# Kernel optimization log

Measured on AMD Instinct MI355X. Metric: run time of the kernel, lower is better.

The kernel has to match this reference:

```python
import jax, jax.numpy as jnp
import numpy as np

N = 50000      # nodes
E = 800000     # edges (avg degree 16)
IN, EMB, HID, OUT = 128, 256, 256, 128
KS = (25000, 12500)  # absolute top-k node counts per pooling level
NEG = -1e9


def setup_inputs() -> dict:
    key = jax.random.key(0)
    k = jax.random.split(key, 20)
    s = 0.05
    rn = lambda kk, shp: (jax.random.normal(kk, shp, jnp.float32) * s)
    return {
        "features": jax.random.normal(k[0], (N, IN), jnp.float32),
        "src": jax.random.randint(k[1], (E,), 0, N, dtype=jnp.int32),
        "dst": jax.random.randint(k[2], (E,), 0, N, dtype=jnp.int32),
        "W_embed": rn(k[3], (IN, EMB)), "b_embed": jnp.zeros((EMB,), jnp.float32),
        "W_enc0": rn(k[4], (EMB, HID)), "b_enc0": jnp.zeros((HID,), jnp.float32),
        "W_enc1": rn(k[5], (HID, HID)), "b_enc1": jnp.zeros((HID,), jnp.float32),
        "W_p0": rn(k[6], (HID, 1)), "b_p0": jnp.zeros((1,), jnp.float32),
        "W_p1": rn(k[7], (HID, 1)), "b_p1": jnp.zeros((1,), jnp.float32),
        "W_bot": rn(k[8], (HID, HID)), "b_bot": jnp.zeros((HID,), jnp.float32),
        "W_dec0": rn(k[9], (HID, HID)), "b_dec0": jnp.zeros((HID,), jnp.float32),
        "W_dec1": rn(k[10], (HID, OUT)), "b_dec1": jnp.zeros((OUT,), jnp.float32),
    }


def _gcn(h, src, dst, emask, W, b, act):
    """DGL GraphConv, norm='both': D_out^{-1/2} A D_in^{-1/2} h W + b, deg clamped >=1.
    emask: float [E] validity mask for edges of the current (sub)graph."""
    n = h.shape[0]
    deg_out = jnp.clip(jax.ops.segment_sum(emask, src, num_segments=n), 1.0)
    deg_in = jnp.clip(jax.ops.segment_sum(emask, dst, num_segments=n), 1.0)
    msg = (h * (deg_out ** -0.5)[:, None])[src] * emask[:, None]  # [E, F]
    agg = jax.ops.segment_sum(msg, dst, num_segments=n)
    out = (agg * (deg_in ** -0.5)[:, None]) @ W + b
    return jax.nn.relu(out) if act else out


def _forward(features, src, dst, W_embed, b_embed, W_enc0, b_enc0, W_enc1, b_enc1,
             W_p0, b_p0, W_p1, b_p1, W_bot, b_bot, W_dec0, b_dec0, W_dec1, b_dec1):
    n = features.shape[0]
    ones_e = jnp.ones((src.shape[0],), features.dtype)
    enc = [(W_enc0, b_enc0), (W_enc1, b_enc1)]
    pools = [(W_p0, b_p0), (W_p1, b_p1)]
    dec = [(W_dec0, b_dec0), (W_dec1, b_dec1)]
    L = len(KS)

    h = _gcn(features, src, dst, ones_e, W_embed, b_embed, True)
    masks = [jnp.ones((n,), features.dtype)]  # node mask per graph level
    hidden = []
    for i in range(L):  # encoder (dropout = eval-mode identity)
        m = masks[i]
        em = m[src] * m[dst]
        h = _gcn(h, src, dst, em, enc[i][0], enc[i][1], True) * m[:, None]
        hidden.append(h)
        # gPool: sigmoid projection score, top-k node selection, gate by score
        scores = jax.nn.sigmoid(h @ pools[i][0] + pools[i][1])[:, 0]
        _, idx = jax.lax.top_k(jnp.where(m > 0, scores, NEG), KS[i])
        nm = jnp.zeros((n,), features.dtype).at[idx].set(1.0)
        h = h * (scores * nm)[:, None]
        masks.append(nm)
    mL = masks[L]
    emL = mL[src] * mL[dst]
    h = _gcn(h, src, dst, emL, W_bot, b_bot, True) * mL[:, None]
    for i in range(L):  # decoder: gUnpool (identity under full-rep masking) + skip + GCN
        j = L - 1 - i
        h = h + hidden[j]
        m = masks[j]
        em = m[src] * m[dst]
        act = i < L - 1  # last decoder layer has no activation
        h = _gcn(h, src, dst, em, dec[i][0], dec[i][1], act) * m[:, None]
    return h


def reference(features, src, dst, W_embed, b_embed, W_enc0, b_enc0, W_enc1, b_enc1,
              W_p0, b_p0, W_p1, b_p1, W_bot, b_bot, W_dec0, b_dec0, W_dec1, b_dec1):
    return _forward(features, src, dst, W_embed, b_embed, W_enc0, b_enc0, W_enc1, b_enc1,
                    W_p0, b_p0, W_p1, b_p1, W_bot, b_bot, W_dec0, b_dec0, W_dec1, b_dec1)
```

## Files before the change

### kernel.cpp

```cpp
#include <hip/hip_runtime.h>
#include <hip/hip_bf16.h>
#include <type_traits>

__global__ void hist_kernel(const int* __restrict__ src, const int* __restrict__ dst,
                            int* __restrict__ deg_out, int* __restrict__ deg_in, int E) {
    int e = blockIdx.x * blockDim.x + threadIdx.x;
    if (e < E) {
        atomicAdd(&deg_out[src[e]], 1);
        atomicAdd(&deg_in[dst[e]], 1);
    }
}

__global__ void scan_kernel(const int* __restrict__ deg, int* __restrict__ row_ptr,
                            int* __restrict__ cursor, int n) {
    __shared__ int wsum[16];
    __shared__ int running;
    int tid = threadIdx.x, lane = tid & 63, wid = tid >> 6;
    if (tid == 0) running = 0;
    __syncthreads();
    for (int base = 0; base < n; base += 1024) {
        int i = base + tid;
        int v = (i < n) ? deg[i] : 0;
        int incl = v;
        #pragma unroll
// ... 93 lines not shown
__device__ __forceinline__ void split4(float x, float y, float z, float w,
                                       ushort4& hv, ushort4& lv) {
    hv.x = f2bf(x); lv.x = f2bf(x - bf2f(hv.x));
    hv.y = f2bf(y); lv.y = f2bf(y - bf2f(hv.y));
    hv.z = f2bf(z); lv.z = f2bf(z - bf2f(hv.z));
    hv.w = f2bf(w); lv.w = f2bf(w - bf2f(hv.w));
}

typedef __attribute__((ext_vector_type(8))) short short8v;
typedef __attribute__((ext_vector_type(4))) float f32x4;

template <bool SPLIT>
__global__ void agg_feat_128_kernel(const int* __restrict__ row_ptr, const int* __restrict__ col,
                                    const float* __restrict__ X, const float* __restrict__ s,
                                    const float* __restrict__ t, float* __restrict__ out,
                                    unsigned short* __restrict__ oh, unsigned short* __restrict__ ol,
                                    int n) {
    int tid = threadIdx.x;
    int node = blockIdx.x * 8 + (tid >> 5);
    int f4 = tid & 31;
    if (node >= n) return;
    int e0 = row_ptr[node], e1 = row_ptr[node + 1];
    const float4* X4 = (const float4*)X;
    float ax = 0.f, ay = 0.f, az = 0.f, aw = 0.f;
    int e = e0;
    for (; e + 3 < e1; e += 4) {
        int u0 = col[e], u1 = col[e + 1], u2 = col[e + 2], u3 = col[e + 3];
        float s0 = s[u0], s1 = s[u1], s2 = s[u2], s3 = s[u3];
        float4 x0 = X4[(size_t)u0 * 32 + f4];
        float4 x1 = X4[(size_t)u1 * 32 + f4];
        float4 x2 = X4[(size_t)u2 * 32 + f4];
        float4 x3 = X4[(size_t)u3 * 32 + f4];
        ax += s0 * x0.x; ay += s0 * x0.y; az += s0 * x0.z; aw += s0 * x0.w;
        ax += s1 * x1.x; ay += s1 * x1.y; az += s1 * x1.z; aw += s1 * x1.w;
        ax += s2 * x2.x; ay += s2 * x2.y; az += s2 * x2.z; aw += s2 * x2.w;
        ax += s3 * x3.x; ay += s3 * x3.y; az += s3 * x3.z; aw += s3 * x3.w;
    }
    for (; e < e1; ++e) {
        int u = col[e];
        float sc = s[u];
        float4 q = X4[(size_t)u * 32 + f4];
        ax += sc * q.x; ay += sc * q.y; az += sc * q.z; aw += sc * q.w;
    }
    float tv = t[node];
    if (SPLIT) {
        ushort4 hv, lv;
        split4(ax * tv, ay * tv, az * tv, aw * tv, hv, lv);
        *(ushort4*)&oh[(size_t)node * 128 + f4 * 4] = hv;
        *(ushort4*)&ol[(size_t)node * 128 + f4 * 4] = lv;
    } else {
        float4 r; r.x = ax * tv; r.y = ay * tv; r.z = az * tv; r.w = aw * tv;
        ((float4*)out)[(size_t)node * 32 + f4] = r;
    }
}

template <bool MASKED, bool SPLIT>
__global__ void agg_f32_256_kernel(const int* __restrict__ row_ptr, const int* __restrict__ col,
                                   const float* __restrict__ X, const float* __restrict__ s,
                                   const float* __restrict__ t, float* __restrict__ out,
                                   unsigned short* __restrict__ oh, unsigned short* __restrict__ ol,
                                   int n) {
    int tid = threadIdx.x;
    int node = blockIdx.x * 4 + (tid >> 6);
    int f4 = tid & 63;
    if (node >= n) return;
    float tv = t[node];
    if (MASKED && tv == 0.f) return;
    int e0 = row_ptr[node], e1 = row_ptr[node + 1];
    const float4* X4 = (const float4*)X;
    float ax = 0.f, ay = 0.f, az = 0.f, aw = 0.f;
    int e = e0;
    for (; e + 3 < e1; e += 4) {
        int u0 = col[e], u1 = col[e + 1], u2 = col[e + 2], u3 = col[e + 3];
        float s0 = s[u0], s1 = s[u1], s2 = s[u2], s3 = s[u3];
        if (!MASKED) {
            float4 x0 = X4[(size_t)u0 * 64 + f4];
            float4 x1 = X4[(size_t)u1 * 64 + f4];
            float4 x2 = X4[(size_t)u2 * 64 + f4];
            float4 x3 = X4[(size_t)u3 * 64 + f4];
            ax += s0 * x0.x; ay += s0 * x0.y; az += s0 * x0.z; aw += s0 * x0.w;
            ax += s1 * x1.x; ay += s1 * x1.y; az += s1 * x1.z; aw += s1 * x1.w;
            ax += s2 * x2.x; ay += s2 * x2.y; az += s2 * x2.z; aw += s2 * x2.w;
            ax += s3 * x3.x; ay += s3 * x3.y; az += s3 * x3.z; aw += s3 * x3.w;
        } else {
            if (s0 != 0.f) { float4 x = X4[(size_t)u0 * 64 + f4];
                ax += s0 * x.x; ay += s0 * x.y; az += s0 * x.z; aw += s0 * x.w; }
            if (s1 != 0.f) { float4 x = X4[(size_t)u1 * 64 + f4];
                ax += s1 * x.x; ay += s1 * x.y; az += s1 * x.z; aw += s1 * x.w; }
            if (s2 != 0.f) { float4 x = X4[(size_t)u2 * 64 + f4];
                ax += s2 * x.x; ay += s2 * x.y; az += s2 * x.z; aw += s2 * x.w; }
            if (s3 != 0.f) { float4 x = X4[(size_t)u3 * 64 + f4];
                ax += s3 * x.x; ay += s3 * x.y; az += s3 * x.z; aw += s3 * x.w; }
        }
    }
    for (; e < e1; ++e) {
        int u = col[e];
        float sc = s[u];
        if (!MASKED || sc != 0.f) {
            float4 xv = X4[(size_t)u * 64 + f4];
            ax += sc * xv.x; ay += sc * xv.y; az += sc * xv.z; aw += sc * xv.w;
        }
    }
    if (SPLIT) {
        ushort4 hv, lv;
        split4(ax * tv, ay * tv, az * tv, aw * tv, hv, lv);
        *(ushort4*)&oh[(size_t)node * 256 + f4 * 4] = hv;
        *(ushort4*)&ol[(size_t)node * 256 + f4 * 4] = lv;
    } else {
        float4 r; r.x = ax * tv; r.y = ay * tv; r.z = az * tv; r.w = aw * tv;
        ((float4*)out)[(size_t)node * 64 + f4] = r;
    }
}

__global__ void agg_bias_128_kernel(const int* __restrict__ row_ptr, const int* __restrict__ col,
                                    const float* __restrict__ P, const float* __restrict__ t,
                                    const float* __restrict__ bias, float* __restrict__ out, int n) {
    int tid = threadIdx.x;
    int node = blockIdx.x * 8 + (tid >> 5);
    int f4 = tid & 31;
    if (node >= n) return;
    int e0 = row_ptr[node], e1 = row_ptr[node + 1];
    const float4* P4 = (const float4*)P;
    float ax = 0.f, ay = 0.f, az = 0.f, aw = 0.f;
    int e = e0;
    for (; e + 3 < e1; e += 4) {
        int u0 = col[e], u1 = col[e + 1], u2 = col[e + 2], u3 = col[e + 3];
        float4 x0 = P4[(size_t)u0 * 32 + f4];
        float4 x1 = P4[(size_t)u1 * 32 + f4];
        float4 x2 = P4[(size_t)u2 * 32 + f4];
        float4 x3 = P4[(size_t)u3 * 32 + f4];
        ax += x0.x; ay += x0.y; az += x0.z; aw += x0.w;
        ax += x1.x; ay += x1.y; az += x1.z; aw += x1.w;
        ax += x2.x; ay += x2.y; az += x2.z; aw += x2.w;
        ax += x3.x; ay += x3.y; az += x3.z; aw += x3.w;
    }
    for (; e < e1; ++e) {
        int u = col[e];
        float4 q = P4[(size_t)u * 32 + f4];
        ax += q.x; ay += q.y; az += q.z; aw += q.w;
    }
    float tv = t[node];
    float4 bv = ((const float4*)bias)[f4];
    float4 r;
    r.x = ax * tv + bv.x; r.y = ay * tv + bv.y;
    r.z = az * tv + bv.z; r.w = aw * tv + bv.w;
    ((float4*)out)[(size_t)node * 32 + f4] = r;
}


__global__ void wsplit_all_kernel(const float* __restrict__ W0, const float* __restrict__ W1,
                                  const float* __restrict__ W2, const float* __restrict__ W3,
                                  const float* __restrict__ W4, const float* __restrict__ W5,
                                  unsigned short* __restrict__ H, unsigned short* __restrict__ L) {
    int i = blockIdx.x * blockDim.x + threadIdx.x;
    const float* W; int rel, base, outIdx;
    if (i < 32768) { W = W0; rel = i; base = 0;
        int k = rel >> 8, nn = rel & 255; outIdx = nn * 128 + k; }
    else if (i < 98304) { W = W1; rel = i - 32768; base = 32768;
        int k = rel >> 8, nn = rel & 255; outIdx = nn * 256 + k; }
    else if (i < 163840) { W = W2; rel = i - 98304; base = 98304;
        int k = rel >> 8, nn = rel & 255; outIdx = nn * 256 + k; }
    else if (i < 229376) { W = W3; rel = i - 163840; base = 163840;
        int k = rel >> 8, nn = rel & 255; outIdx = nn * 256 + k; }
    else if (i < 294912) { W = W4; rel = i - 229376; base = 229376;
        int k = rel >> 8, nn = rel & 255; outIdx = nn * 256 + k; }
    else { W = W5; rel = i - 294912; base = 294912;
        int k = rel >> 7, nn = rel & 127; outIdx = nn * 256 + k; }
    float x = W[rel];
    unsigned short h = f2bf(x);
    H[base + outIdx] = h;
    L[base + outIdx] = f2bf(x - bf2f(h));
}

template <bool RELU>
__global__ __launch_bounds__(256, 3) void gemm_mfma_kernel(
    const unsigned short* __restrict__ Ah, const unsigned short* __restrict__ Al,
    const unsigned short* __restrict__ Wh, const unsigned short* __restrict__ Wl,
    const float* __restrict__ bias, float* __restrict__ C, int M, int K, int Nn) {
    __shared__ __align__(16) short sAh[128][40];
    __shared__ __align__(16) short sAl[128][40];
    __shared__ __align__(16) short sWh[128][40];
    __shared__ __align__(16) short sWl[128][40];
    int tid = threadIdx.x;
    int bm = blockIdx.x * 128, bn = blockIdx.y * 128;
    int lane = tid & 63, wid = tid >> 6;
    int wr = (wid >> 1) * 64, wc = (wid & 1) * 64;
    int lr = lane & 15, kg = lane >> 4;
    int arow = tid >> 1, akq = (tid & 1) * 16;
    const unsigned short* ahp = Ah + (size_t)(bm + arow) * K + akq;
    const unsigned short* alp = Al + (size_t)(bm + arow) * K + akq;
    const unsigned short* whp = Wh + (size_t)(bn + arow) * K + akq;
    const unsigned short* wlp = Wl + (size_t)(bn + arow) * K + akq;
    f32x4 acc[4][4];
    #pragma unroll
    for (int i = 0; i < 4; ++i)
        #pragma unroll
        for (int j = 0; j < 4; ++j) acc[i][j] = (f32x4){0.f, 0.f, 0.f, 0.f};
    for (int k0 = 0; k0 < K; k0 += 32) {
        short8v a0 = *(const short8v*)(ahp + k0);
        short8v a1 = *(const short8v*)(ahp + k0 + 8);
        short8v l0 = *(const short8v*)(alp + k0);
        short8v l1 = *(const short8v*)(alp + k0 + 8);
        short8v w0 = *(const short8v*)(whp + k0);
        short8v w1 = *(const short8v*)(whp + k0 + 8);
        short8v v0 = *(const short8v*)(wlp + k0);
        short8v v1 = *(const short8v*)(wlp + k0 + 8);
        __syncthreads();
        *(short8v*)&sAh[arow][akq] = a0; *(short8v*)&sAh[arow][akq + 8] = a1;
        *(short8v*)&sAl[arow][akq] = l0; *(short8v*)&sAl[arow][akq + 8] = l1;
        *(short8v*)&sWh[arow][akq] = w0; *(short8v*)&sWh[arow][akq + 8] = w1;
        *(short8v*)&sWl[arow][akq] = v0; *(short8v*)&sWl[arow][akq + 8] = v1;
        __syncthreads();
        short8v ah[4], al[4];
        #pragma unroll
        for (int mf = 0; mf < 4; ++mf) {
            ah[mf] = *(const short8v*)&sAh[wr + mf * 16 + lr][kg * 8];
            al[mf] = *(const short8v*)&sAl[wr + mf * 16 + lr][kg * 8];
        }
        #pragma unroll
        for (int nf = 0; nf < 4; ++nf) {
            short8v bh = *(const short8v*)&sWh[wc + nf * 16 + lr][kg * 8];
            short8v bl = *(const short8v*)&sWl[wc + nf * 16 + lr][kg * 8];
            #pragma unroll
            for (int mf = 0; mf < 4; ++mf) {
                acc[mf][nf] = __builtin_amdgcn_mfma_f32_16x16x32_bf16(ah[mf], bh, acc[mf][nf], 0, 0, 0);
                acc[mf][nf] = __builtin_amdgcn_mfma_f32_16x16x32_bf16(ah[mf], bl, acc[mf][nf], 0, 0, 0);
                acc[mf][nf] = __builtin_amdgcn_mfma_f32_16x16x32_bf16(al[mf], bh, acc[mf][nf], 0, 0, 0);
            }
        }
    }
    #pragma unroll
    for (int mf = 0; mf < 4; ++mf) {
        #pragma unroll
        for (int nf = 0; nf < 4; ++nf) {
            int col = bn + wc + nf * 16 + lr;
            float bv = bias ? bias[col] : 0.f;
            #pragma unroll
            for (int r = 0; r < 4; ++r) {
                int grow = bm + wr + mf * 16 + kg * 4 + r;
                if (grow < M) {
                    float x = acc[mf][nf][r] + bv;
                    if (RELU) x = fmaxf(x, 0.f);
                    C[(size_t)grow * Nn + col] = x;
                }
            }
        }
    }
}

template <bool RELU>
__global__ __launch_bounds__(256, 3) void gemm_rows_mfma_kernel(
    const unsigned short* __restrict__ Ah, const unsigned short* __restrict__ Al,
    const unsigned short* __restrict__ Wh, const unsigned short* __restrict__ Wl,
    const float* __restrict__ bias, const int* __restrict__ idx, int Mc,
    float* __restrict__ C, int K, int Nn) {
    __shared__ __align__(16) short sAh[128][40];
    __shared__ __align__(16) short sAl[128][40];
    __shared__ __align__(16) short sWh[128][40];
    __shared__ __align__(16) short sWl[128][40];
    __shared__ int ridx[128];
    int tid = threadIdx.x;
    int bm = blockIdx.x * 128, bn = blockIdx.y * 128;
    int lane = tid & 63, wid = tid >> 6;
    int wr = (wid >> 1) * 64, wc = (wid & 1) * 64;
    int lr = lane & 15, kg = lane >> 4;
    int arow = tid >> 1, akq = (tid & 1) * 16;
    if (tid < 128) {
        int r = bm + tid;
        ridx[tid] = (r < Mc) ? idx[r] : idx[0];
    }
    __syncthreads();
    int rA = ridx[arow];
    const unsigned short* ahp = Ah + (size_t)rA * K + akq;
    const unsigned short* alp = Al + (size_t)rA * K + akq;
    const unsigned short* whp = Wh + (size_t)(bn + arow) * K + akq;
    const unsigned short* wlp = Wl + (size_t)(bn + arow) * K + akq;
    f32x4 acc[4][4];
    #pragma unroll
    for (int i = 0; i < 4; ++i)
        #pragma unroll
        for (int j = 0; j < 4; ++j) acc[i][j] = (f32x4){0.f, 0.f, 0.f, 0.f};
    for (int k0 = 0; k0 < K; k0 += 32) {
        short8v a0 = *(const short8v*)(ahp + k0);
        short8v a1 = *(const short8v*)(ahp + k0 + 8);
        short8v l0 = *(const short8v*)(alp + k0);
        short8v l1 = *(const short8v*)(alp + k0 + 8);
        short8v w0 = *(const short8v*)(whp + k0);
        short8v w1 = *(const short8v*)(whp + k0 + 8);
        short8v v0 = *(const short8v*)(wlp + k0);
        short8v v1 = *(const short8v*)(wlp + k0 + 8);
        __syncthreads();
        *(short8v*)&sAh[arow][akq] = a0; *(short8v*)&sAh[arow][akq + 8] = a1;
        *(short8v*)&sAl[arow][akq] = l0; *(short8v*)&sAl[arow][akq + 8] = l1;
        *(short8v*)&sWh[arow][akq] = w0; *(short8v*)&sWh[arow][akq + 8] = w1;
        *(short8v*)&sWl[arow][akq] = v0; *(short8v*)&sWl[arow][akq + 8] = v1;
        __syncthreads();
        short8v ah[4], al[4];
        #pragma unroll
        for (int mf = 0; mf < 4; ++mf) {
            ah[mf] = *(const short8v*)&sAh[wr + mf * 16 + lr][kg * 8];
            al[mf] = *(const short8v*)&sAl[wr + mf * 16 + lr][kg * 8];
        }
        #pragma unroll
        for (int nf = 0; nf < 4; ++nf) {
            short8v bh = *(const short8v*)&sWh[wc + nf * 16 + lr][kg * 8];
            short8v bl = *(const short8v*)&sWl[wc + nf * 16 + lr][kg * 8];
            #pragma unroll
            for (int mf = 0; mf < 4; ++mf) {
                acc[mf][nf] = __builtin_amdgcn_mfma_f32_16x16x32_bf16(ah[mf], bh, acc[mf][nf], 0, 0, 0);
                acc[mf][nf] = __builtin_amdgcn_mfma_f32_16x16x32_bf16(ah[mf], bl, acc[mf][nf], 0, 0, 0);
                acc[mf][nf] = __builtin_amdgcn_mfma_f32_16x16x32_bf16(al[mf], bh, acc[mf][nf], 0, 0, 0);
            }
        }
    }
    #pragma unroll
    for (int mf = 0; mf < 4; ++mf) {
        #pragma unroll
        for (int nf = 0; nf < 4; ++nf) {
            int col = bn + wc + nf * 16 + lr;
            float bv = bias[col];
            #pragma unroll
            for (int r = 0; r < 4; ++r) {
                int lrow = wr + mf * 16 + kg * 4 + r;
                if (bm + lrow < Mc) {
                    int grow = ridx[lrow];
                    float x = acc[mf][nf][r] + bv;
                    if (RELU) x = fmaxf(x, 0.f);
                    C[(size_t)grow * Nn + col] = x;
                }
            }
        }
    }
}

__global__ __launch_bounds__(256, 3) void gemm_dec1_kernel(
    const float* __restrict__ A, const float* __restrict__ B,
    const float* __restrict__ mask, const float* __restrict__ rs,
    const unsigned short* __restrict__ Wh, const unsigned short* __restrict__ Wl,
    float* __restrict__ C, int M, int K) {
    __shared__ __align__(16) short sAh[128][40];
    __shared__ __align__(16) short sAl[128][40];
    __shared__ __align__(16) short sWh[128][40];
    __shared__ __align__(16) short sWl[128][40];
    const int Nn = 128;
    int tid = threadIdx.x;
    int bm = blockIdx.x * 128, bn = 0;
    int lane = tid & 63, wid = tid >> 6;
    int wr = (wid >> 1) * 64, wc = (wid & 1) * 64;
    int lr = lane & 15, kg = lane >> 4;
    int arow = tid >> 1, akq = (tid & 1) * 16;
    float mv = (mask[bm + arow] != 0.f) ? 1.f : 0.f;
    float rsv = rs[bm + arow];
    const float* apf = A + (size_t)(bm + arow) * K + akq;
    const float* bpf = B + (size_t)(bm + arow) * K + akq;
    const unsigned short* whp = Wh + (size_t)(bn + arow) * K + akq;
    const unsigned short* wlp = Wl + (size_t)(bn + arow) * K + akq;
    f32x4 acc[4][4];
    #pragma unroll
    for (int i = 0; i < 4; ++i)
        #pragma unroll
        for (int j = 0; j < 4; ++j) acc[i][j] = (f32x4){0.f, 0.f, 0.f, 0.f};
    for (int k0 = 0; k0 < K; k0 += 32) {
        const float4* pa = (const float4*)(apf + k0);
        const float4* pb = (const float4*)(bpf + k0);
        float4 qa0 = pa[0], qa1 = pa[1], qa2 = pa[2], qa3 = pa[3];
        float4 qb0 = pb[0], qb1 = pb[1], qb2 = pb[2], qb3 = pb[3];
        ushort4 h0, l0v, h1, l1v, h2, l2v, h3, l3v;
        split4((qa0.x * mv + qb0.x) * rsv, (qa0.y * mv + qb0.y) * rsv,
               (qa0.z * mv + qb0.z) * rsv, (qa0.w * mv + qb0.w) * rsv, h0, l0v);
        split4((qa1.x * mv + qb1.x) * rsv, (qa1.y * mv + qb1.y) * rsv,
               (qa1.z * mv + qb1.z) * rsv, (qa1.w * mv + qb1.w) * rsv, h1, l1v);
        split4((qa2.x * mv + qb2.x) * rsv, (qa2.y * mv + qb2.y) * rsv,
               (qa2.z * mv + qb2.z) * rsv, (qa2.w * mv + qb2.w) * rsv, h2, l2v);
        split4((qa3.x * mv + qb3.x) * rsv, (qa3.y * mv + qb3.y) * rsv,
               (qa3.z * mv + qb3.z) * rsv, (qa3.w * mv + qb3.w) * rsv, h3, l3v);
        short8v w0 = *(const short8v*)(whp + k0);
        short8v w1 = *(const short8v*)(whp + k0 + 8);
        short8v v0 = *(const short8v*)(wlp + k0);
        short8v v1 = *(const short8v*)(wlp + k0 + 8);
        __syncthreads();
        *(ushort4*)&sAh[arow][akq]      = h0; *(ushort4*)&sAh[arow][akq + 4]  = h1;
        *(ushort4*)&sAh[arow][akq + 8]  = h2; *(ushort4*)&sAh[arow][akq + 12] = h3;
        *(ushort4*)&sAl[arow][akq]      = l0v; *(ushort4*)&sAl[arow][akq + 4]  = l1v;
        *(ushort4*)&sAl[arow][akq + 8]  = l2v; *(ushort4*)&sAl[arow][akq + 12] = l3v;
        *(short8v*)&sWh[arow][akq] = w0; *(short8v*)&sWh[arow][akq + 8] = w1;
        *(short8v*)&sWl[arow][akq] = v0; *(short8v*)&sWl[arow][akq + 8] = v1;
        __syncthreads();
        short8v ah[4], al[4];
        #pragma unroll
        for (int mf = 0; mf < 4; ++mf) {
            ah[mf] = *(const short8v*)&sAh[wr + mf * 16 + lr][kg * 8];
            al[mf] = *(const short8v*)&sAl[wr + mf * 16 + lr][kg * 8];
        }
        #pragma unroll
        for (int nf = 0; nf < 4; ++nf) {
            short8v bh = *(const short8v*)&sWh[wc + nf * 16 + lr][kg * 8];
            short8v bl = *(const short8v*)&sWl[wc + nf * 16 + lr][kg * 8];
            #pragma unroll
            for (int mf = 0; mf < 4; ++mf) {
                acc[mf][nf] = __builtin_amdgcn_mfma_f32_16x16x32_bf16(ah[mf], bh, acc[mf][nf], 0, 0, 0);
                acc[mf][nf] = __builtin_amdgcn_mfma_f32_16x16x32_bf16(ah[mf], bl, acc[mf][nf], 0, 0, 0);
                acc[mf][nf] = __builtin_amdgcn_mfma_f32_16x16x32_bf16(al[mf], bh, acc[mf][nf], 0, 0, 0);
            }
        }
    }
    #pragma unroll
    for (int mf = 0; mf < 4; ++mf) {
        #pragma unroll
        for (int nf = 0; nf < 4; ++nf) {
            int col = bn + wc + nf * 16 + lr;
            #pragma unroll
            for (int r = 0; r < 4; ++r) {
                int grow = bm + wr + mf * 16 + kg * 4 + r;
                if (grow < M) C[(size_t)grow * Nn + col] = acc[mf][nf][r];
            }
        }
    }
}

template <bool RELU>
__global__ __launch_bounds__(256) void gemm_kernel(const float* __restrict__ A,
                                                   const float* __restrict__ W,
                                                   const float* __restrict__ bias,
                                                   const float* __restrict__ mask,
                                                   const float* __restrict__ rowscale,
                                                   float* __restrict__ C, int M, int K, int Nn) {
    __shared__ float As[16][68];
    __shared__ float Bs[16][132];
    int tid = threadIdx.x;
    int bm = blockIdx.x * 64, bn = blockIdx.y * 128;
    int mA = tid >> 2, kqA = (tid & 3) * 4;
    int kB = tid >> 4, nqB = (tid & 15) * 8;
    int tm = (tid >> 4) * 4, tn = (tid & 15) * 4;
    float acc[4][8] = {};
    float rs = rowscale ? rowscale[bm + mA] : 1.f;
    for (int k0 = 0; k0 < K; k0 += 16) {
        float4 av = *(const float4*)(A + (size_t)(bm + mA) * K + k0 + kqA);
        As[kqA + 0][mA] = av.x * rs; As[kqA + 1][mA] = av.y * rs;
        As[kqA + 2][mA] = av.z * rs; As[kqA + 3][mA] = av.w * rs;
        const float* wp = W + (size_t)(k0 + kB) * Nn + bn + nqB;
        *(float4*)&Bs[kB][nqB]     = *(const float4*)wp;
        *(float4*)&Bs[kB][nqB + 4] = *(const float4*)(wp + 4);
        __syncthreads();
        #pragma unroll
        for (int kk = 0; kk < 16; ++kk) {
            float4 a  = *(const float4*)&As[kk][tm];
            float4 b0 = *(const float4*)&Bs[kk][tn];
            float4 b1 = *(const float4*)&Bs[kk][tn + 64];
            float ar[4] = {a.x, a.y, a.z, a.w};
            float br[8] = {b0.x, b0.y, b0.z, b0.w, b1.x, b1.y, b1.z, b1.w};
            #pragma unroll
            for (int i2 = 0; i2 < 4; i2++)
                #pragma unroll
                for (int j = 0; j < 8; j++) acc[i2][j] += ar[i2] * br[j];
        }
        __syncthreads();
    }
    #pragma unroll
    for (int i2 = 0; i2 < 4; i2++) {
        int row = bm + tm + i2;
        if (row < M) {
            float mv = mask ? mask[row] : 1.f;
            float o[8];
            #pragma unroll
            for (int j = 0; j < 8; j++) {
                int cj = (j < 4) ? (tn + j) : (64 + tn + j - 4);
                float x = acc[i2][j] + (bias ? bias[bn + cj] : 0.f);
                if (RELU) x = fmaxf(x, 0.f);
                o[j] = x * mv;
            }
            float* cp = C + (size_t)row * Nn + bn;
            *(float4*)(cp + tn)      = make_float4(o[0], o[1], o[2], o[3]);
            *(float4*)(cp + 64 + tn) = make_float4(o[4], o[5], o[6], o[7]);
        }
    }
}

__global__ void score_kernel(const float* __restrict__ H, const float* __restrict__ Wp,
                             const float* __restrict__ bp, const float* __restrict__ mask,
                             float* __restrict__ scores, float* __restrict__ keys, int n) {
    int lane = threadIdx.x & 63;
    int node = blockIdx.x * 4 + (threadIdx.x >> 6);
    if (node >= n) return;
    float4 hv = ((const float4*)(H + (size_t)node * 256))[lane];
    float4 wq = ((const float4*)Wp)[lane];
    float d = hv.x * wq.x + hv.y * wq.y + hv.z * wq.z + hv.w * wq.w;
    #pragma unroll
    for (int off = 32; off > 0; off >>= 1) d += __shfl_down(d, off);
    if (lane == 0) {
        float sc = 1.f / (1.f + expf(-(d + bp[0])));
        scores[node] = sc;
        keys[node] = (mask && mask[node] == 0.f) ? -1e9f : sc;
    }
}

__device__ __forceinline__ unsigned key_u(float f) {
    unsigned u = __float_as_uint(f);
    return (u & 0x80000000u) ? ~u : (u | 0x80000000u);
}

__device__ __forceinline__ void wave_hist_add(int* __restrict__ hist, unsigned bin, bool valid) {
    int lane = threadIdx.x & 63;
    while (true) {
        unsigned long long vmask = __ballot(valid);
        if (vmask == 0ull) break;
        int leader = __ffsll((long long)vmask) - 1;
        unsigned lbin = (unsigned)__shfl((int)bin, leader);
        bool match = valid && (bin == lbin);
        unsigned long long mmask = __ballot(match);
        if (lane == leader) atomicAdd(&hist[lbin], __popcll(mmask));
        if (match) valid = false;
    }
}

__global__ void topk_kernel(const float* __restrict__ keys, const float* __restrict__ scores,
                            float* __restrict__ nm, float* __restrict__ gate, int n, int K) {
    __shared__ int hist[256];
    __shared__ unsigned sh_prefix;
    __shared__ int sh_krem;
    __shared__ int sh_running;
    __shared__ int wsum[16];
    int tid = threadIdx.x, lane = tid & 63, wid = tid >> 6;
    if (tid == 0) { sh_prefix = 0u; sh_krem = K; sh_running = 0; }
    __syncthreads();
    for (int pass = 0; pass < 4; ++pass) {
        int shift = 24 - pass * 8;
        if (tid < 256) hist[tid] = 0;
        __syncthreads();
        unsigned pmask = (pass == 0) ? 0u : (0xFFFFFFFFu << (shift + 8));
        unsigned prefix = sh_prefix;
        for (int i = tid; i < n; i += 1024) {
            unsigned u = key_u(keys[i]);
            if ((u & pmask) == prefix) atomicAdd(&hist[(u >> shift) & 0xFF], 1);
        }
        __syncthreads();
        if (tid == 0) {
            int krem = sh_krem;
// ... 110 lines not shown
            }
            run += c;
        }
    }
}

__global__ void topk_mark(const float* __restrict__ keys, const float* __restrict__ scores,
                          const int* __restrict__ sel, float* __restrict__ nm,
                          float* __restrict__ gate, int* __restrict__ tie_list,
                          int* __restrict__ tie_cnt, int n) {
    int i = blockIdx.x * blockDim.x + threadIdx.x;
    if (i >= n) return;
    unsigned Tkey = (unsigned)sel[2];
    unsigned u = key_u(keys[i]);
    float v = 0.f;
    if (u > Tkey) v = 1.f;
    else if (u == Tkey) { int p = atomicAdd(tie_cnt, 1); tie_list[p] = i; }
    nm[i] = v;
    gate[i] = v * scores[i];
}

__global__ void topk_ties(const float* __restrict__ scores, const int* __restrict__ sel,
                          const int* __restrict__ tie_list, const int* __restrict__ tie_cnt,
                          float* __restrict__ nm, float* __restrict__ gate) {
    int cnt = *tie_cnt;
    int need = sel[3];
    for (int j = threadIdx.x; j < cnt; j += blockDim.x) {
        int idx = tie_list[j];
        int rank = 0;
        for (int k2 = 0; k2 < cnt; ++k2) rank += (tie_list[k2] < idx) ? 1 : 0;
        if (rank < need) { nm[idx] = 1.f; gate[idx] = scores[idx]; }
    }
}

__global__ void compact_kernel(const float* __restrict__ nm, int* __restrict__ idx,
                               int* __restrict__ cnt, int n) {
    int i = blockIdx.x * blockDim.x + threadIdx.x;
    if (i < n && nm[i] != 0.f) {
        int p = atomicAdd(cnt, 1);
        idx[p] = i;
    }
}

__global__ void add_mask_kernel(float* __restrict__ A, const float* __restrict__ B,
                                const float* __restrict__ mask, int n4) {
    int i = blockIdx.x * blockDim.x + threadIdx.x;
    if (i < n4) {
        float4 a = ((float4*)A)[i];
        float4 b = ((const float4*)B)[i];
        if (mask && mask[i >> 6] == 0.f) { a.x = 0.f; a.y = 0.f; a.z = 0.f; a.w = 0.f; }
        a.x += b.x; a.y += b.y; a.z += b.z; a.w += b.w;
        ((float4*)A)[i] = a;
    }
}

extern "C" void kernel_launch(void* const* d_in, const int* in_sizes, int n_in,
                              void* d_out, int out_size, void* d_ws, size_t ws_size,
                              hipStream_t stream) {
    const int n = in_sizes[0] / 128;
    const int E = in_sizes[1];
    const int NPAD = ((n + 127) / 128) * 128;
    const int K1 = 25000, K2 = 12500;

    const float* features = (const float*)d_in[0];
    const int* src = (const int*)d_in[1];
    const int* dst = (const int*)d_in[2];
    const float* W_embed = (const float*)d_in[3];
    const float* b_embed = (const float*)d_in[4];
    const float* W_enc0  = (const float*)d_in[5];
    const float* b_enc0  = (const float*)d_in[6];
    const float* W_enc1  = (const float*)d_in[7];
    const float* b_enc1  = (const float*)d_in[8];
    const float* W_p0    = (const float*)d_in[9];
    const float* b_p0    = (const float*)d_in[10];
    const float* W_p1    = (const float*)d_in[11];
    const float* b_p1    = (const float*)d_in[12];
    const float* W_bot   = (const float*)d_in[13];
    const float* b_bot   = (const float*)d_in[14];
    const float* W_dec0  = (const float*)d_in[15];
    const float* b_dec0  = (const float*)d_in[16];
    const float* W_dec1  = (const float*)d_in[17];
    const float* b_dec1  = (const float*)d_in[18];
    float* out_f = (float*)d_out;

    char* ws = (char*)d_ws;
    size_t off = 0;
    auto alloc = [&](size_t bytes) -> void* {
        void* p = ws + off;
        off += (bytes + 255) & ~(size_t)255;
        return p;
    };
    (void)alloc(256);
    int* row_ptr  = (int*)alloc((size_t)(n + 1) * 4);
    int* cursor   = (int*)alloc((size_t)n * 4);
    int* col      = (int*)alloc((size_t)E * 4);
    int* deg_out_i= (int*)alloc((size_t)n * 4);
    int* deg_in_i = (int*)alloc((size_t)n * 4);
    float* so_m1  = (float*)alloc((size_t)n * 4);
    float* si_m1  = (float*)alloc((size_t)n * 4);
    float* so_m2  = (float*)alloc((size_t)n * 4);
    float* si_m2  = (float*)alloc((size_t)n * 4);
    float* sarr   = (float*)alloc((size_t)n * 4);
    float* tarr   = (float*)alloc((size_t)n * 4);
    float* scores1= (float*)alloc((size_t)n * 4);
    float* keys1  = (float*)alloc((size_t)n * 4);
    float* scores2= (float*)alloc((size_t)n * 4);
    float* keys2  = (float*)alloc((size_t)n * 4);
    float* nm1    = (float*)alloc((size_t)n * 4);
    float* gate1  = (float*)alloc((size_t)n * 4);
    float* nm2    = (float*)alloc((size_t)n * 4);
    float* gate2  = (float*)alloc((size_t)n * 4);
    size_t big = (size_t)NPAD * 256 * 4;
    float* A = (float*)alloc(big);
    float* B = (float*)alloc(big);
    float* C = (float*)alloc(big);
    float* D = (float*)alloc(big);
    unsigned short* Dh = (unsigned short*)D;
    unsigned short* Dl = Dh + (size_t)NPAD * 256;
    unsigned short* Dh128 = Dh;
    unsigned short* Dl128 = Dh + (size_t)NPAD * 128;
    int* rhist    = (int*)alloc(65536 * 4);
    int* sel      = (int*)alloc(256);
    int* tie_cnt  = (int*)alloc(256);
    int* tie_list = (int*)alloc((size_t)n * 4);
    float* s0     = (float*)alloc((size_t)n * 4);
    float* t0     = (float*)alloc((size_t)n * 4);
    int* idx1     = (int*)alloc((size_t)n * 4);
    int* idx2     = (int*)alloc((size_t)n * 4);
    int* ccnt     = (int*)alloc(256);
    const int WO_EMBED = 0, WO_ENC0 = 32768, WO_ENC1 = 98304,
              WO_BOT = 163840, WO_DEC0 = 229376, WO_DEC1 = 294912;
    const int WTOT = 327680;
    unsigned short* wsph = (unsigned short*)alloc((size_t)WTOT * 2);
    unsigned short* wspl = (unsigned short*)alloc((size_t)WTOT * 2);
    bool fast = (off <= ws_size);

    dim3 blk(256);
    int gE = (E + 255) / 256;
    int gN = (n + 255) / 256;
    int gAgg256 = (n + 3) / 4;
    int gAgg128 = (n + 7) / 8;
    int gScore = (n + 3) / 4;
    dim3 gemm_g(NPAD / 128, 2);
    dim3 gemm_g128(NPAD / 128, 1);
    dim3 gemm_gK1((K1 + 127) / 128, 2);
    dim3 gemm_gK2((K2 + 127) / 128, 2);
    dim3 gemm_gv(NPAD / 64, 2);
    dim3 gemm_gv128(NPAD / 64, 1);
    int gAdd = (n * 64 + 255) / 256;

    auto run_topk = [&](const float* keys, const float* scores, float* nm, float* gate, int K) {
        if (fast) {
            hipMemsetAsync(rhist, 0, 65536 * 4, stream);
            topk_hist1<<<gN, blk, 0, stream>>>(keys, n, rhist);
            topk_scan1<<<1, 1024, 0, stream>>>(rhist, K, sel);
            hipMemsetAsync(rhist, 0, 65536 * 4, stream);
            topk_hist2<<<gN, blk, 0, stream>>>(keys, n, sel, rhist);
            topk_scan2<<<1, 1024, 0, stream>>>(rhist, sel, tie_cnt);
            topk_mark<<<gN, blk, 0, stream>>>(keys, scores, sel, nm, gate, tie_list, tie_cnt, n);
            topk_ties<<<1, 256, 0, stream>>>(scores, sel, tie_list, tie_cnt, nm, gate);
        } else {
            topk_kernel<<<1, 1024, 0, stream>>>(keys, scores, nm, gate, n, K);
        }
    };
    float* sF = fast ? s0 : sarr;
    float* tF = fast ? t0 : tarr;

    if (fast) {
        wsplit_all_kernel<<<WTOT / 256, blk, 0, stream>>>(W_embed, W_enc0, W_enc1, W_bot,
                                                          W_dec0, W_dec1, wsph, wspl);
    }

    {
        size_t degpad = (((size_t)n * 4) + 255) & ~(size_t)255;
        hipMemsetAsync(deg_out_i, 0, degpad + (size_t)n * 4, stream);
    }
    hist_kernel<<<gE, blk, 0, stream>>>(src, dst, deg_out_i, deg_in_i, E);
    scan_kernel<<<1, 1024, 0, stream>>>(deg_in_i, row_ptr, cursor, n);
    fill_kernel<<<gE, blk, 0, stream>>>(src, dst, cursor, col, E);
    sort_rows_kernel<<<gN, blk, 0, stream>>>(row_ptr, col, n);

    scale_full_kernel<<<gN, blk, 0, stream>>>(deg_out_i, deg_in_i, sF, tF, n);

    if (fast) {
        agg_feat_128_kernel<true><<<gAgg128, blk, 0, stream>>>(row_ptr, col, features, sF, tF,
                                                               nullptr, Dh128, Dl128, n);
        gemm_mfma_kernel<true><<<gemm_g, blk, 0, stream>>>(Dh128, Dl128, wsph + WO_EMBED,
                                                           wspl + WO_EMBED, b_embed, A, n, 128, 256);
    } else {
        agg_feat_128_kernel<false><<<gAgg128, blk, 0, stream>>>(row_ptr, col, features, sF, tF,
                                                                D, nullptr, nullptr, n);
        gemm_kernel<true><<<gemm_gv, blk, 0, stream>>>(D, W_embed, b_embed, nullptr, nullptr, A, n, 128, 256);
    }

    if (fast) {
        agg_f32_256_kernel<false, true><<<gAgg256, blk, 0, stream>>>(row_ptr, col, A, sF, tF,
                                                                     nullptr, Dh, Dl, n);
        gemm_mfma_kernel<true><<<gemm_g, blk, 0, stream>>>(Dh, Dl, wsph + WO_ENC0, wspl + WO_ENC0,
                                                           b_enc0, B, n, 256, 256);
    } else {
        agg_f32_256_kernel<false, false><<<gAgg256, blk, 0, stream>>>(row_ptr, col, A, sF, tF,
                                                                      D, nullptr, nullptr, n);
        gemm_kernel<true><<<gemm_gv, blk, 0, stream>>>(D, W_enc0, b_enc0, nullptr, nullptr, B, n, 256, 256);
    }

    score_kernel<<<gScore, blk, 0, stream>>>(B, W_p0, b_p0, nullptr, scores1, keys1, n);
    run_topk(keys1, scores1, nm1, gate1, K1);
    if (fast) {
        hipMemsetAsync(ccnt, 0, 4, stream);
        compact_kernel<<<gN, blk, 0, stream>>>(nm1, idx1, ccnt, n);
    }

    hipMemsetAsync(so_m1, 0, (size_t)n * 4, stream);
    out_deg_mask_kernel<<<gE, blk, 0, stream>>>(src, dst, nm1, so_m1, E);
    in_deg_mask_kernel<<<gN, blk, 0, stream>>>(row_ptr, col, nm1, si_m1, n);
    scale_mask_kernel<<<gN, blk, 0, stream>>>(gate1, nm1, so_m1, si_m1, sarr, tarr, n);
    if (fast) {
        agg_f32_256_kernel<true, true><<<gAgg256, blk, 0, stream>>>(row_ptr, col, B, sarr, tarr,
                                                                    nullptr, Dh, Dl, n);
        gemm_rows_mfma_kernel<true><<<gemm_gK1, blk, 0, stream>>>(Dh, Dl, wsph + WO_ENC1,
                                                                  wspl + WO_ENC1, b_enc1, idx1, K1, C, 256, 256);
    } else {
        agg_f32_256_kernel<true, false><<<gAgg256, blk, 0, stream>>>(row_ptr, col, B, sarr, tarr,
                                                                     D, nullptr, nullptr, n);
        gemm_kernel<true><<<gemm_gv, blk, 0, stream>>>(D, W_enc1, b_enc1, nm1, nullptr, C, n, 256, 256);
    }

    score_kernel<<<gScore, blk, 0, stream>>>(C, W_p1, b_p1, nm1, scores2, keys2, n);
    run_topk(keys2, scores2, nm2, gate2, K2);
    if (fast) {
        hipMemsetAsync(ccnt + 1, 0, 4, stream);
        compact_kernel<<<gN, blk, 0, stream>>>(nm2, idx2, ccnt + 1, n);
    }

    hipMemsetAsync(so_m2, 0, (size_t)n * 4, stream);
    out_deg_mask_kernel<<<gE, blk, 0, stream>>>(src, dst, nm2, so_m2, E);
    in_deg_mask_kernel<<<gN, blk, 0, stream>>>(row_ptr, col, nm2, si_m2, n);
    scale_mask_kernel<<<gN, blk, 0, stream>>>(gate2, nm2, so_m2, si_m2, sarr, tarr, n);
    if (fast) {
        agg_f32_256_kernel<true, true><<<gAgg256, blk, 0, stream>>>(row_ptr, col, C, sarr, tarr,
                                                                    nullptr, Dh, Dl, n);
        gemm_rows_mfma_kernel<true><<<gemm_gK2, blk, 0, stream>>>(Dh, Dl, wsph + WO_BOT,
                                                                  wspl + WO_BOT, b_bot, idx2, K2, A, 256, 256);
    } else {
        agg_f32_256_kernel<true, false><<<gAgg256, blk, 0, stream>>>(row_ptr, col, C, sarr, tarr,
                                                                     D, nullptr, nullptr, n);
        gemm_kernel<true><<<gemm_gv, blk, 0, stream>>>(D, W_bot, b_bot, nm2, nullptr, A, n, 256, 256);
    }

    add_mask_kernel<<<gAdd, blk, 0, stream>>>(A, C, fast ? nm2 : nullptr, n * 64);
    scale_mask_kernel<<<gN, blk, 0, stream>>>(nm1, nm1, so_m1, si_m1, sarr, tarr, n);
    if (fast) {
        agg_f32_256_kernel<true, true><<<gAgg256, blk, 0, stream>>>(row_ptr, col, A, sarr, tarr,
                                                                    nullptr, Dh, Dl, n);
        gemm_rows_mfma_kernel<true><<<gemm_gK1, blk, 0, stream>>>(Dh, Dl, wsph + WO_DEC0,
                                                                  wspl + WO_DEC0, b_dec0, idx1, K1, A, 256, 256);
    } else {
        agg_f32_256_kernel<true, false><<<gAgg256, blk, 0, stream>>>(row_ptr, col, A, sarr, tarr,
                                                                     D, nullptr, nullptr, n);
        gemm_kernel<true><<<gemm_gv, blk, 0, stream>>>(D, W_dec0, b_dec0, nm1, nullptr, A, n, 256, 256);
    }

    if (fast) {
        gemm_dec1_kernel<<<gemm_g128, blk, 0, stream>>>(A, B, nm1, sF, wsph + WO_DEC1,
                                                        wspl + WO_DEC1, C, n, 256);
    } else {
        add_mask_kernel<<<gAdd, blk, 0, stream>>>(A, B, nullptr, n * 64);
        scale_full_kernel<<<gN, blk, 0, stream>>>(deg_out_i, deg_in_i, sarr, tarr, n);
        gemm_kernel<false><<<gemm_gv128, blk, 0, stream>>>(A, W_dec1, nullptr, nullptr, sF, C, n, 256, 128);
    }
    agg_bias_128_kernel<<<gAgg128, blk, 0, stream>>>(row_ptr, col, C, tF, b_dec1, out_f, n);

    (void)n_in; (void)out_size;
}
```

Baseline: 1.143 ms.

## Store 256-wide activations in feature-chunked column-major layout for cache-local gathers

GEMM epilogues now write 256-wide activations as 16 chunks of 16 features, each chunk laid out contiguously across all padded nodes. A new aggregation kernel assigns each block one chunk, with the low bits of the block index selecting the chunk so chunks spread across XCDs. The point is that the neighbour gather per chunk touches only a few MB and can stay resident in L2 instead of streaming full rows. The score, add-mask and dec1 GEMM input paths are adapted to read the chunked layout. The risks are four-lane-wide 64-byte gathers per node, uncoalesced strided column stores in the GEMM epilogues, and nontemporal hints on the col index loads.

```diff
diff --git a/kernel.cpp b/kernel.cpp
--- a/kernel.cpp
+++ b/kernel.cpp
@@ -169,6 +169,69 @@
         float4 r; r.x = ax * tv; r.y = ay * tv; r.z = az * tv; r.w = aw * tv;
         ((float4*)out)[(size_t)node * 32 + f4] = r;
     }
+}
+
+template <bool MASKED>
+__global__ void agg_cm_256_kernel(const int* __restrict__ row_ptr, const int* __restrict__ col,
+                                  const float* __restrict__ Xcm, const float* __restrict__ s,
+                                  const float* __restrict__ t,
+                                  unsigned short* __restrict__ oh, unsigned short* __restrict__ ol,
+                                  int n, int NPAD, int G) {
+    int tid = threadIdx.x;
+    int bid = blockIdx.x;
+    int x = bid & 7;
+    int rest = bid >> 3;
+    int p = rest / G;
+    int g = rest - p * G;
+    int chunk = p * 8 + x;
+    int node = g * 64 + (tid >> 2);
+    int q = tid & 3;
+    if (node >= n) return;
+    float tv = t[node];
+    if (MASKED && tv == 0.f) return;
+    int e0 = row_ptr[node], e1 = row_ptr[node + 1];
+    const float4* Xc = (const float4*)Xcm + (size_t)chunk * NPAD * 4 + q;
+    float ax = 0.f, ay = 0.f, az = 0.f, aw = 0.f;
+    int e = e0;
+    for (; e + 3 < e1; e += 4) {
+        int u0 = __builtin_nontemporal_load(&col[e]);
+        int u1 = __builtin_nontemporal_load(&col[e + 1]);
+        int u2 = __builtin_nontemporal_load(&col[e + 2]);
+        int u3 = __builtin_nontemporal_load(&col[e + 3]);
+        float s0 = s[u0], s1 = s[u1], s2 = s[u2], s3 = s[u3];
+        if (!MASKED) {
+            float4 x0 = Xc[(size_t)u0 * 4];
+            float4 x1 = Xc[(size_t)u1 * 4];
+            float4 x2 = Xc[(size_t)u2 * 4];
+            float4 x3 = Xc[(size_t)u3 * 4];
+            ax += s0 * x0.x; ay += s0 * x0.y; az += s0 * x0.z; aw += s0 * x0.w;
+            ax += s1 * x1.x; ay += s1 * x1.y; az += s1 * x1.z; aw += s1 * x1.w;
+            ax += s2 * x2.x; ay += s2 * x2.y; az += s2 * x2.z; aw += s2 * x2.w;
+            ax += s3 * x3.x; ay += s3 * x3.y; az += s3 * x3.z; aw += s3 * x3.w;
+        } else {
+            if (s0 != 0.f) { float4 v = Xc[(size_t)u0 * 4];
+                ax += s0 * v.x; ay += s0 * v.y; az += s0 * v.z; aw += s0 * v.w; }
+            if (s1 != 0.f) { float4 v = Xc[(size_t)u1 * 4];
+                ax += s1 * v.x; ay += s1 * v.y; az += s1 * v.z; aw += s1 * v.w; }
+            if (s2 != 0.f) { float4 v = Xc[(size_t)u2 * 4];
+                ax += s2 * v.x; ay += s2 * v.y; az += s2 * v.z; aw += s2 * v.w; }
+            if (s3 != 0.f) { float4 v = Xc[(size_t)u3 * 4];
+                ax += s3 * v.x; ay += s3 * v.y; az += s3 * v.z; aw += s3 * v.w; }
+        }
+    }
+    for (; e < e1; ++e) {
+        int u = __builtin_nontemporal_load(&col[e]);
+        float sc = s[u];
+        if (!MASKED || sc != 0.f) {
+            float4 v = Xc[(size_t)u * 4];
+            ax += sc * v.x; ay += sc * v.y; az += sc * v.z; aw += sc * v.w;
+        }
+    }
+    ushort4 hv, lv;
+    split4(ax * tv, ay * tv, az * tv, aw * tv, hv, lv);
+    size_t o = (size_t)node * 256 + chunk * 16 + q * 4;
+    __builtin_nontemporal_store(*(const unsigned long long*)&hv, (unsigned long long*)&oh[o]);
+    __builtin_nontemporal_store(*(const unsigned long long*)&lv, (unsigned long long*)&ol[o]);
 }
 
 template <bool MASKED, bool SPLIT>
@@ -200,14 +263,14 @@
             ax += s2 * x2.x; ay += s2 * x2.y; az += s2 * x2.z; aw += s2 * x2.w;
             ax += s3 * x3.x; ay += s3 * x3.y; az += s3 * x3.z; aw += s3 * x3.w;
         } else {
-            if (s0 != 0.f) { float4 x = X4[(size_t)u0 * 64 + f4];
-                ax += s0 * x.x; ay += s0 * x.y; az += s0 * x.z; aw += s0 * x.w; }
-            if (s1 != 0.f) { float4 x = X4[(size_t)u1 * 64 + f4];
-                ax += s1 * x.x; ay += s1 * x.y; az += s1 * x.z; aw += s1 * x.w; }
-            if (s2 != 0.f) { float4 x = X4[(size_t)u2 * 64 + f4];
-                ax += s2 * x.x; ay += s2 * x.y; az += s2 * x.z; aw += s2 * x.w; }
-            if (s3 != 0.f) { float4 x = X4[(size_t)u3 * 64 + f4];
-                ax += s3 * x.x; ay += s3 * x.y; az += s3 * x.z; aw += s3 * x.w; }
+            if (s0 != 0.f) { float4 v = X4[(size_t)u0 * 64 + f4];
+                ax += s0 * v.x; ay += s0 * v.y; az += s0 * v.z; aw += s0 * v.w; }
+            if (s1 != 0.f) { float4 v = X4[(size_t)u1 * 64 + f4];
+                ax += s1 * v.x; ay += s1 * v.y; az += s1 * v.z; aw += s1 * v.w; }
+            if (s2 != 0.f) { float4 v = X4[(size_t)u2 * 64 + f4];
+                ax += s2 * v.x; ay += s2 * v.y; az += s2 * v.z; aw += s2 * v.w; }
+            if (s3 != 0.f) { float4 v = X4[(size_t)u3 * 64 + f4];
+                ax += s3 * v.x; ay += s3 * v.y; az += s3 * v.z; aw += s3 * v.w; }
         }
     }
     for (; e < e1; ++e) {
@@ -293,7 +356,7 @@
 __global__ __launch_bounds__(256, 3) void gemm_mfma_kernel(
     const unsigned short* __restrict__ Ah, const unsigned short* __restrict__ Al,
     const unsigned short* __restrict__ Wh, const unsigned short* __restrict__ Wl,
-    const float* __restrict__ bias, float* __restrict__ C, int M, int K, int Nn) {
+    const float* __restrict__ bias, float* __restrict__ C, int M, int K, int NPAD) {
     __shared__ __align__(16) short sAh[128][40];
     __shared__ __align__(16) short sAl[128][40];
     __shared__ __align__(16) short sWh[128][40];
@@ -350,15 +413,17 @@
     for (int mf = 0; mf < 4; ++mf) {
         #pragma unroll
         for (int nf = 0; nf < 4; ++nf) {
-            int col = bn + wc + nf * 16 + lr;
-            float bv = bias ? bias[col] : 0.f;
+            int colg = bn + wc + nf * 16 + lr;
+            int ck = colg >> 4, cw = colg & 15;
+            float bv = bias ? bias[colg] : 0.f;
+            float* cbase = C + (size_t)ck * NPAD * 16 + cw;
             #pragma unroll
             for (int r = 0; r < 4; ++r) {
                 int grow = bm + wr + mf * 16 + kg * 4 + r;
                 if (grow < M) {
                     float x = acc[mf][nf][r] + bv;
                     if (RELU) x = fmaxf(x, 0.f);
-                    C[(size_t)grow * Nn + col] = x;
+                    cbase[(size_t)grow * 16] = x;
                 }
             }
         }
@@ -370,7 +435,7 @@
     const unsigned short* __restrict__ Ah, const unsigned short* __restrict__ Al,
     const unsigned short* __restrict__ Wh, const unsigned short* __restrict__ Wl,
     const float* __restrict__ bias, const int* __restrict__ idx, int Mc,
-    float* __restrict__ C, int K, int Nn) {
+    float* __restrict__ C, int K, int NPAD) {
     __shared__ __align__(16) short sAh[128][40];
     __shared__ __align__(16) short sAl[128][40];
     __shared__ __align__(16) short sWh[128][40];
@@ -434,8 +499,10 @@
     for (int mf = 0; mf < 4; ++mf) {
         #pragma unroll
         for (int nf = 0; nf < 4; ++nf) {
-            int col = bn + wc + nf * 16 + lr;
-            float bv = bias[col];
+            int colg = bn + wc + nf * 16 + lr;
+            int ck = colg >> 4, cw = colg & 15;
+            float bv = bias[colg];
+            float* cbase = C + (size_t)ck * NPAD * 16 + cw;
             #pragma unroll
             for (int r = 0; r < 4; ++r) {
                 int lrow = wr + mf * 16 + kg * 4 + r;
@@ -443,7 +510,7 @@
                     int grow = ridx[lrow];
                     float x = acc[mf][nf][r] + bv;
                     if (RELU) x = fmaxf(x, 0.f);
-                    C[(size_t)grow * Nn + col] = x;
+                    cbase[(size_t)grow * 16] = x;
                 }
             }
         }
@@ -454,7 +521,7 @@
     const float* __restrict__ A, const float* __restrict__ B,
     const float* __restrict__ mask, const float* __restrict__ rs,
     const unsigned short* __restrict__ Wh, const unsigned short* __restrict__ Wl,
-    float* __restrict__ C, int M, int K) {
+    float* __restrict__ C, int M, int K, int NPAD) {
     __shared__ __align__(16) short sAh[128][40];
     __shared__ __align__(16) short sAl[128][40];
     __shared__ __align__(16) short sWh[128][40];
@@ -468,8 +535,6 @@
     int arow = tid >> 1, akq = (tid & 1) * 16;
     float mv = (mask[bm + arow] != 0.f) ? 1.f : 0.f;
     float rsv = rs[bm + arow];
-    const float* apf = A + (size_t)(bm + arow) * K + akq;
-    const float* bpf = B + (size_t)(bm + arow) * K + akq;
     const unsigned short* whp = Wh + (size_t)(bn + arow) * K + akq;
     const unsigned short* wlp = Wl + (size_t)(bn + arow) * K + akq;
     f32x4 acc[4][4];
@@ -478,8 +543,9 @@
         #pragma unroll
         for (int j = 0; j < 4; ++j) acc[i][j] = (f32x4){0.f, 0.f, 0.f, 0.f};
     for (int k0 = 0; k0 < K; k0 += 32) {
-        const float4* pa = (const float4*)(apf + k0);
-        const float4* pb = (const float4*)(bpf + k0);
+        int ck = (k0 + akq) >> 4;
+        const float4* pa = (const float4*)A + ((size_t)ck * NPAD + bm + arow) * 4;
+        const float4* pb = (const float4*)B + ((size_t)ck * NPAD + bm + arow) * 4;
         float4 qa0 = pa[0], qa1 = pa[1], qa2 = pa[2], qa3 = pa[3];
         float4 qb0 = pb[0], qb1 = pb[1], qb2 = pb[2], qb3 = pb[3];
         ushort4 h0, l0v, h1, l1v, h2, l2v, h3, l3v;
@@ -525,11 +591,11 @@
     for (int mf = 0; mf < 4; ++mf) {
         #pragma unroll
         for (int nf = 0; nf < 4; ++nf) {
-            int col = bn + wc + nf * 16 + lr;
+            int colg = bn + wc + nf * 16 + lr;
             #pragma unroll
             for (int r = 0; r < 4; ++r) {
                 int grow = bm + wr + mf * 16 + kg * 4 + r;
-                if (grow < M) C[(size_t)grow * Nn + col] = acc[mf][nf][r];
+                if (grow < M) C[(size_t)grow * Nn + colg] = acc[mf][nf][r];
             }
         }
     }
@@ -593,13 +659,21 @@
     }
 }
 
+template <bool CM>
 __global__ void score_kernel(const float* __restrict__ H, const float* __restrict__ Wp,
                              const float* __restrict__ bp, const float* __restrict__ mask,
-                             float* __restrict__ scores, float* __restrict__ keys, int n) {
+                             float* __restrict__ scores, float* __restrict__ keys,
+                             int n, int NPAD) {
     int lane = threadIdx.x & 63;
     int node = blockIdx.x * 4 + (threadIdx.x >> 6);
     if (node >= n) return;
-    float4 hv = ((const float4*)(H + (size_t)node * 256))[lane];
+    float4 hv;
+    if (CM) {
+        int c = lane >> 2, q = lane & 3;
+        hv = ((const float4*)H)[((size_t)c * NPAD + node) * 4 + q];
+    } else {
+        hv = ((const float4*)(H + (size_t)node * 256))[lane];
+    }
     float4 wq = ((const float4*)Wp)[lane];
     float d = hv.x * wq.x + hv.y * wq.y + hv.z * wq.z + hv.w * wq.w;
     #pragma unroll
@@ -816,6 +890,23 @@
         a.x += b.x; a.y += b.y; a.z += b.z; a.w += b.w;
         ((float4*)A)[i] = a;
     }
+}
+
+__global__ void add_mask_cm_kernel(float* __restrict__ A, const float* __restrict__ B,
+                                   const float* __restrict__ mask, int n, int NPAD) {
+    int i = blockIdx.x * blockDim.x + threadIdx.x;
+    int per = n * 4;
+    int total = 16 * per;
+    if (i >= total) return;
+    int c = i / per;
+    int w = i - c * per;
+    int node = w >> 2;
+    size_t a4 = (size_t)c * NPAD * 4 + w;
+    float4 a = ((float4*)A)[a4];
+    float4 b = ((const float4*)B)[a4];
+    if (mask[node] == 0.f) { a.x = 0.f; a.y = 0.f; a.z = 0.f; a.w = 0.f; }
+    a.x += b.x; a.y += b.y; a.z += b.z; a.w += b.w;
+    ((float4*)A)[a4] = a;
 }
 
 extern "C" void kernel_launch(void* const* d_in, const int* in_sizes, int n_in,
@@ -902,6 +993,8 @@
     dim3 blk(256);
     int gE = (E + 255) / 256;
     int gN = (n + 255) / 256;
+    int Gcm = (n + 63) / 64;
+    int gAggCM = 2 * Gcm * 8;
     int gAgg256 = (n + 3) / 4;
     int gAgg128 = (n + 7) / 8;
     int gScore = (n + 3) / 4;
@@ -912,6 +1005,7 @@
     dim3 gemm_gv(NPAD / 64, 2);
     dim3 gemm_gv128(NPAD / 64, 1);
     int gAdd = (n * 64 + 255) / 256;
+    int gAddCM = (16 * n * 4 + 255) / 256;
 
     auto run_topk = [&](const float* keys, const float* scores, float* nm, float* gate, int K) {
         if (fast) {
@@ -950,7 +1044,7 @@
         agg_feat_128_kernel<true><<<gAgg128, blk, 0, stream>>>(row_ptr, col, features, sF, tF,
                                                                nullptr, Dh128, Dl128, n);
         gemm_mfma_kernel<true><<<gemm_g, blk, 0, stream>>>(Dh128, Dl128, wsph + WO_EMBED,
-                                                           wspl + WO_EMBED, b_embed, A, n, 128, 256);
+                                                           wspl + WO_EMBED, b_embed, A, n, 128, NPAD);
     } else {
         agg_feat_128_kernel<false><<<gAgg128, blk, 0, stream>>>(row_ptr, col, features, sF, tF,
                                                                 D, nullptr, nullptr, n);
@@ -958,17 +1052,20 @@
     }
 
     if (fast) {
-        agg_f32_256_kernel<false, true><<<gAgg256, blk, 0, stream>>>(row_ptr, col, A, sF, tF,
-                                                                     nullptr, Dh, Dl, n);
+        agg_cm_256_kernel<false><<<gAggCM, blk, 0, stream>>>(row_ptr, col, A, sF, tF,
+                                                             Dh, Dl, n, NPAD, Gcm);
         gemm_mfma_kernel<true><<<gemm_g, blk, 0, stream>>>(Dh, Dl, wsph + WO_ENC0, wspl + WO_ENC0,
-                                                           b_enc0, B, n, 256, 256);
+                                                           b_enc0, B, n, 256, NPAD);
     } else {
         agg_f32_256_kernel<false, false><<<gAgg256, blk, 0, stream>>>(row_ptr, col, A, sF, tF,
                                                                       D, nullptr, nullptr, n);
         gemm_kernel<true><<<gemm_gv, blk, 0, stream>>>(D, W_enc0, b_enc0, nullptr, nullptr, B, n, 256, 256);
     }
 
-    score_kernel<<<gScore, blk, 0, stream>>>(B, W_p0, b_p0, nullptr, scores1, keys1, n);
+    if (fast)
+        score_kernel<true><<<gScore, blk, 0, stream>>>(B, W_p0, b_p0, nullptr, scores1, keys1, n, NPAD);
+    else
+        score_kernel<false><<<gScore, blk, 0, stream>>>(B, W_p0, b_p0, nullptr, scores1, keys1, n, NPAD);
     run_topk(keys1, scores1, nm1, gate1, K1);
     if (fast) {
         hipMemsetAsync(ccnt, 0, 4, stream);
@@ -980,17 +1077,20 @@
     in_deg_mask_kernel<<<gN, blk, 0, stream>>>(row_ptr, col, nm1, si_m1, n);
     scale_mask_kernel<<<gN, blk, 0, stream>>>(gate1, nm1, so_m1, si_m1, sarr, tarr, n);
     if (fast) {
-        agg_f32_256_kernel<true, true><<<gAgg256, blk, 0, stream>>>(row_ptr, col, B, sarr, tarr,
-                                                                    nullptr, Dh, Dl, n);
+        agg_cm_256_kernel<true><<<gAggCM, blk, 0, stream>>>(row_ptr, col, B, sarr, tarr,
+                                                            Dh, Dl, n, NPAD, Gcm);
         gemm_rows_mfma_kernel<true><<<gemm_gK1, blk, 0, stream>>>(Dh, Dl, wsph + WO_ENC1,
-                                                                  wspl + WO_ENC1, b_enc1, idx1, K1, C, 256, 256);
+                                                                  wspl + WO_ENC1, b_enc1, idx1, K1, C, 256, NPAD);
     } else {
         agg_f32_256_kernel<true, false><<<gAgg256, blk, 0, stream>>>(row_ptr, col, B, sarr, tarr,
                                                                      D, nullptr, nullptr, n);
         gemm_kernel<true><<<gemm_gv, blk, 0, stream>>>(D, W_enc1, b_enc1, nm1, nullptr, C, n, 256, 256);
     }
 
-    score_kernel<<<gScore, blk, 0, stream>>>(C, W_p1, b_p1, nm1, scores2, keys2, n);
+    if (fast)
+        score_kernel<true><<<gScore, blk, 0, stream>>>(C, W_p1, b_p1, nm1, scores2, keys2, n, NPAD);
+    else
+        score_kernel<false><<<gScore, blk, 0, stream>>>(C, W_p1, b_p1, nm1, scores2, keys2, n, NPAD);
     run_topk(keys2, scores2, nm2, gate2, K2);
     if (fast) {
         hipMemsetAsync(ccnt + 1, 0, 4, stream);
@@ -1002,23 +1102,26 @@
     in_deg_mask_kernel<<<gN, blk, 0, stream>>>(row_ptr, col, nm2, si_m2, n);
     scale_mask_kernel<<<gN, blk, 0, stream>>>(gate2, nm2, so_m2, si_m2, sarr, tarr, n);
     if (fast) {
-        agg_f32_256_kernel<true, true><<<gAgg256, blk, 0, stream>>>(row_ptr, col, C, sarr, tarr,
-                                                                    nullptr, Dh, Dl, n);
+        agg_cm_256_kernel<true><<<gAggCM, blk, 0, stream>>>(row_ptr, col, C, sarr, tarr,
+                                                            Dh, Dl, n, NPAD, Gcm);
         gemm_rows_mfma_kernel<true><<<gemm_gK2, blk, 0, stream>>>(Dh, Dl, wsph + WO_BOT,
-                                                                  wspl + WO_BOT, b_bot, idx2, K2, A, 256, 256);
+                                                                  wspl + WO_BOT, b_bot, idx2, K2, A, 256, NPAD);
     } else {
         agg_f32_256_kernel<true, false><<<gAgg256, blk, 0, stream>>>(row_ptr, col, C, sarr, tarr,
                                                                      D, nullptr, nullptr, n);
         gemm_kernel<true><<<gemm_gv, blk, 0, stream>>>(D, W_bot, b_bot, nm2, nullptr, A, n, 256, 256);
     }
 
-    add_mask_kernel<<<gAdd, blk, 0, stream>>>(A, C, fast ? nm2 : nullptr, n * 64);
+    if (fast)
+        add_mask_cm_kernel<<<gAddCM, blk, 0, stream>>>(A, C, nm2, n, NPAD);
+    else
+        add_mask_kernel<<<gAdd, blk, 0, stream>>>(A, C, nullptr, n * 64);
     scale_mask_kernel<<<gN, blk, 0, stream>>>(nm1, nm1, so_m1, si_m1, sarr, tarr, n);
     if (fast) {
-        agg_f32_256_kernel<true, true><<<gAgg256, blk, 0, stream>>>(row_ptr, col, A, sarr, tarr,
-                                                                    nullptr, Dh, Dl, n);
+        agg_cm_256_kernel<true><<<gAggCM, blk, 0, stream>>>(row_ptr, col, A, sarr, tarr,
+                                                            Dh, Dl, n, NPAD, Gcm);
         gemm_rows_mfma_kernel<true><<<gemm_gK1, blk, 0, stream>>>(Dh, Dl, wsph + WO_DEC0,
-                                                                  wspl + WO_DEC0, b_dec0, idx1, K1, A, 256, 256);
+                                                                  wspl + WO_DEC0, b_dec0, idx1, K1, A, 256, NPAD);
     } else {
         agg_f32_256_kernel<true, false><<<gAgg256, blk, 0, stream>>>(row_ptr, col, A, sarr, tarr,
                                                                      D, nullptr, nullptr, n);
@@ -1027,7 +1130,7 @@
 
     if (fast) {
         gemm_dec1_kernel<<<gemm_g128, blk, 0, stream>>>(A, B, nm1, sF, wsph + WO_DEC1,
-                                                        wspl + WO_DEC1, C, n, 256);
+                                                        wspl + WO_DEC1, C, n, 256, NPAD);
     } else {
         add_mask_kernel<<<gAdd, blk, 0, stream>>>(A, B, nullptr, n * 64);
         scale_full_kernel<<<gN, blk, 0, stream>>>(deg_out_i, deg_in_i, sarr, tarr, n);
```

After: 1.602 ms. 40.2% more time.
